# Kernel optimization log

Hardware: AMD Instinct MI355X
Metric: run time of the kernel (lower is better)

## Reference

```python
import jax, jax.numpy as jnp
import numpy as np

NUM_EXPERTS = 64
TOP_K = 2

def setup_inputs() -> dict:
    key = jax.random.key(0)
    k1, k2, k3, k4 = jax.random.split(key, 4)
    B, N, C, E = 4, 4096, 2048, NUM_EXPERTS
    x = jax.random.normal(k1, (B, N, C), dtype=jnp.float32)
    routing_context = jax.random.normal(k2, (B, C), dtype=jnp.float32)
    # Linear(C, E, bias=False) and Linear(C, C, bias=False), torch layout (out, in)
    gate_w = jax.random.normal(k3, (E, C), dtype=jnp.float32) * (1.0 / np.sqrt(C))
    ctx_w = jax.random.normal(k4, (C, C), dtype=jnp.float32) * (1.0 / np.sqrt(C))
    return {"x": x, "routing_context": routing_context, "gate_w": gate_w, "ctx_w": ctx_w}

def reference(x, routing_context, gate_w, ctx_w):
    B, N, C = x.shape
    T = B * N
    E = gate_w.shape[0]
    # context_proj(routing_context): (B,C) @ (C,C)^T -> broadcast over N
    ctx = routing_context @ ctx_w.T                      # (B, C)
    x_routing = (x + ctx[:, None, :]).reshape(T, C)      # (T, C)
    logits = x_routing @ gate_w.T                        # (T, E)
    top_vals, top_idx = jax.lax.top_k(logits, TOP_K)     # (T, K) each
    top_weights = jax.nn.softmax(top_vals, axis=-1)      # (T, K)
    probs = jax.nn.softmax(logits, axis=-1)              # (T, E)
    importance = probs.sum(axis=0) / T                   # (E,)
    # load: fraction of tokens that pick each expert in their top-k
    load = jnp.zeros((E,), dtype=probs.dtype).at[top_idx.reshape(-1)].add(1.0) / T
    aux_loss = E * (importance * load).sum()
    return top_idx, top_weights, aux_loss
```

## Files before the change

### kernel.cpp

```cpp
#include <hip/hip_runtime.h>
#include <math.h>

#define T_TOKENS 16384
#define C_DIM    2048
#define N_SEQ    4096
#define E_EXP    64
#define NSLICE   4
#define KSLICE   512
#define EPB      1024
#define GN       131072

typedef __attribute__((ext_vector_type(8))) short  short8;
typedef __attribute__((ext_vector_type(4))) float  floatx4;

__device__ __forceinline__ void splitv(float v, ushort& h, ushort& m, ushort& l) {
    unsigned u = __float_as_uint(v);
    h = (ushort)(u >> 16);
    float f1 = v - __uint_as_float(u & 0xffff0000u);
    unsigned u1 = __float_as_uint(f1);
    m = (ushort)(u1 >> 16);
    float f2 = f1 - __uint_as_float(u1 & 0xffff0000u);
    l = (ushort)(__float_as_uint(f2) >> 16);
}

__device__ __forceinline__ void splitpack8(const float4& a, const float4& b,
                                           short8& h, short8& m, short8& l) {
    ushort hh, mm, ll;
    splitv(a.x, hh, mm, ll); h[0] = hh; m[0] = mm; l[0] = ll;
    splitv(a.y, hh, mm, ll); h[1] = hh; m[1] = mm; l[1] = ll;
    splitv(a.z, hh, mm, ll); h[2] = hh; m[2] = mm; l[2] = ll;
    splitv(a.w, hh, mm, ll); h[3] = hh; m[3] = mm; l[3] = ll;
    splitv(b.x, hh, mm, ll); h[4] = hh; m[4] = mm; l[4] = ll;
    splitv(b.y, hh, mm, ll); h[5] = hh; m[5] = mm; l[5] = ll;
    splitv(b.z, hh, mm, ll); h[6] = hh; m[6] = mm; l[6] = ll;
    splitv(b.w, hh, mm, ll); h[7] = hh; m[7] = mm; l[7] = ll;
}

__device__ __forceinline__ void split3rne(float v, ushort& h, ushort& m, ushort& l) {
    unsigned u = __float_as_uint(v);
    unsigned r = (u + 0x7fffu + ((u >> 16) & 1u)) >> 16;
    h = (ushort)r;
    float e1 = v - __uint_as_float(r << 16);
    u = __float_as_uint(e1);
    r = (u + 0x7fffu + ((u >> 16) & 1u)) >> 16;
    m = (ushort)r;
    float e2 = e1 - __uint_as_float(r << 16);
    l = (ushort)(__float_as_uint(e2) >> 16);
}

__global__ __launch_bounds__(256) void ctx_kernel(
    const float* __restrict__ rc, const float* __restrict__ ctx_w,
    float* __restrict__ ctx_out)
{
    const int w    = threadIdx.x >> 6;
    const int lane = threadIdx.x & 63;
    const int o    = blockIdx.x * 4 + w;
    const int b    = o >> 11;
    const int j    = o & 2047;

    const float4* wr = (const float4*)(ctx_w + (size_t)j * C_DIM);
    const float4* rr = (const float4*)(rc + (size_t)b * C_DIM);
    float s = 0.f;
#pragma unroll
    for (int it = 0; it < 8; ++it) {
        float4 a = wr[it * 64 + lane];
        float4 c = rr[it * 64 + lane];
        s += a.x * c.x + a.y * c.y + a.z * c.z + a.w * c.w;
    }
#pragma unroll
    for (int off = 32; off; off >>= 1) s += __shfl_xor(s, off, 64);
    if (lane == 0) ctx_out[b * C_DIM + j] = s;
}

__global__ __launch_bounds__(256) void prep_kernel(
    const float* __restrict__ gw, const float* __restrict__ ctx,
    ushort* __restrict__ gsp, float* __restrict__ cl)
{
    if (blockIdx.x < 512) {
        const int idx  = blockIdx.x * 256 + threadIdx.x;
        const int j    = idx & 7;
        const int e    = (idx >> 3) & 63;
        const int koct = idx >> 9;
        float g = gw[(size_t)e * C_DIM + koct * 8 + j];
        ushort h, m, l;
        split3rne(g, h, m, l);
        gsp[idx]          = h;
        gsp[GN + idx]     = m;
        gsp[2 * GN + idx] = l;
    } else {
        const int lane = threadIdx.x & 63;
        const int pk   = (blockIdx.x - 512) * 4 + (threadIdx.x >> 6);
        const int b    = pk >> 6;
        const int e    = pk & 63;
        const float4* wr = (const float4*)(gw + (size_t)e * C_DIM);
        const float4* cr = (const float4*)(ctx + (size_t)b * C_DIM);
        float s = 0.f;
#pragma unroll
        for (int it = 0; it < 8; ++it) {
            float4 a = wr[it * 64 + lane];
            float4 c = cr[it * 64 + lane];
            s += a.x * c.x + a.y * c.y + a.z * c.z + a.w * c.w;
        }
#pragma unroll
        for (int off = 32; off; off >>= 1) s += __shfl_xor(s, off, 64);
        if (lane == 0) cl[pk] = s;
    }
}

__global__ __launch_bounds__(256) void gemm_mfma_kernel(
    const float* __restrict__ x, const ushort* __restrict__ gsp,
    float* __restrict__ P)
{
    const int tid   = threadIdx.x;
    const int wv    = tid >> 6;
    const int lane  = tid & 63;
    const int l15   = lane & 15;
    const int quad  = lane >> 4;
    const int tile  = blockIdx.x & 127;
    const int slice = blockIdx.x >> 7;
    const int tw    = tile * 128 + wv * 32;
    const int cbase = slice * KSLICE;

    floatx4 acc[2][4];
#pragma unroll
    for (int s = 0; s < 2; ++s)
#pragma unroll
        for (int nt = 0; nt < 4; ++nt) acc[s][nt] = (floatx4){0.f, 0.f, 0.f, 0.f};

    const float* xr0 = x + (size_t)(tw + l15) * C_DIM + cbase + quad * 8;
    const float* xr1 = xr0 + (size_t)16 * C_DIM;
    const ushort* bb = gsp + ((size_t)((cbase >> 3) + quad) * 64 + l15) * 8;

#pragma unroll 2
    for (int ks = 0; ks < KSLICE / 32; ++ks) {
        float4 a00 = *(const float4*)(xr0 + ks * 32);
        float4 a01 = *(const float4*)(xr0 + ks * 32 + 4);
        float4 a10 = *(const float4*)(xr1 + ks * 32);
        float4 a11 = *(const float4*)(xr1 + ks * 32 + 4);
        short8 ah0, am0, al0, ah1, am1, al1;
        splitpack8(a00, a01, ah0, am0, al0);
        splitpack8(a10, a11, ah1, am1, al1);

        const ushort* bks = bb + (size_t)ks * 4 * 64 * 8;
#pragma unroll
        for (int nt = 0; nt < 4; ++nt) {
            const ushort* bp_ = bks + (size_t)(16 * nt) * 8;
            short8 bh = *(const short8*)(bp_);
            short8 bm = *(const short8*)(bp_ + GN);
            short8 bl = *(const short8*)(bp_ + 2 * (size_t)GN);
            acc[0][nt] = __builtin_amdgcn_mfma_f32_16x16x32_bf16(ah0, bh, acc[0][nt], 0, 0, 0);
            acc[0][nt] = __builtin_amdgcn_mfma_f32_16x16x32_bf16(ah0, bm, acc[0][nt], 0, 0, 0);
            acc[0][nt] = __builtin_amdgcn_mfma_f32_16x16x32_bf16(am0, bh, acc[0][nt], 0, 0, 0);
            acc[0][nt] = __builtin_amdgcn_mfma_f32_16x16x32_bf16(ah0, bl, acc[0][nt], 0, 0, 0);
            acc[0][nt] = __builtin_amdgcn_mfma_f32_16x16x32_bf16(al0, bh, acc[0][nt], 0, 0, 0);
            acc[0][nt] = __builtin_amdgcn_mfma_f32_16x16x32_bf16(am0, bm, acc[0][nt], 0, 0, 0);
            acc[1][nt] = __builtin_amdgcn_mfma_f32_16x16x32_bf16(ah1, bh, acc[1][nt], 0, 0, 0);
            acc[1][nt] = __builtin_amdgcn_mfma_f32_16x16x32_bf16(ah1, bm, acc[1][nt], 0, 0, 0);
            acc[1][nt] = __builtin_amdgcn_mfma_f32_16x16x32_bf16(am1, bh, acc[1][nt], 0, 0, 0);
            acc[1][nt] = __builtin_amdgcn_mfma_f32_16x16x32_bf16(ah1, bl, acc[1][nt], 0, 0, 0);
            acc[1][nt] = __builtin_amdgcn_mfma_f32_16x16x32_bf16(al1, bh, acc[1][nt], 0, 0, 0);
            acc[1][nt] = __builtin_amdgcn_mfma_f32_16x16x32_bf16(am1, bm, acc[1][nt], 0, 0, 0);
        }
    }

    float* Ps = P + ((size_t)slice * T_TOKENS + tw) * E_EXP;
#pragma unroll
    for (int s = 0; s < 2; ++s)
#pragma unroll
        for (int nt = 0; nt < 4; ++nt)
#pragma unroll
            for (int r = 0; r < 4; ++r)
                Ps[(size_t)(s * 16 + quad * 4 + r) * E_EXP + 16 * nt + l15] =
                    acc[s][nt][r];
}

__global__ __launch_bounds__(256) void epilogue_kernel(
    const float* __restrict__ P, const float* __restrict__ cl,
    float* __restrict__ out, float* __restrict__ bp)
{
    __shared__ float red[4][128];

    const int tid  = threadIdx.x;
    const int wv   = tid >> 6;
    const int lane = tid & 63;
    const int t0   = blockIdx.x * (T_TOKENS / EPB);
    const float clv = cl[(t0 >> 12) * 64 + lane];

    float imp_acc = 0.f, cnt_acc = 0.f;

    for (int tt = 0; tt < 4; ++tt) {
        const int t = t0 + wv * 4 + tt;
        float v = clv;
#pragma unroll
        for (int s = 0; s < NSLICE; ++s)
            v += P[((size_t)s * T_TOKENS + t) * E_EXP + lane];

        const float p = expf(v);
        float v1 = v;  int i1 = lane;
        float v2 = -INFINITY; int i2 = 0x7fffffff;
        float s = p;
#pragma unroll
        for (int off = 32; off; off >>= 1) {
            float ov1 = __shfl_xor(v1, off, 64);
            int   oi1 = __shfl_xor(i1, off, 64);
            float ov2 = __shfl_xor(v2, off, 64);
            int   oi2 = __shfl_xor(i2, off, 64);
            s += __shfl_xor(s, off, 64);
            const bool aw = (ov1 < v1) || (ov1 == v1 && i1 < oi1);
            const float lv = aw ? ov1 : v1;  const int li = aw ? oi1 : i1;
            const float wv2 = aw ? v2 : ov2; const int wi = aw ? i2 : oi2;
            if (!aw) { v1 = ov1; i1 = oi1; }
            const bool sw = (wv2 < lv) || (wv2 == lv && li < wi);
            v2 = sw ? lv : wv2; i2 = sw ? li : wi;
        }

        imp_acc += p / s;
        if (lane == i1 || lane == i2) cnt_acc += 1.f;

        if (lane == 0) {
            const float e2 = expf(v2 - v1);
            out[2 * t]     = (float)i1;
            out[2 * t + 1] = (float)i2;
            out[2 * T_TOKENS + 2 * t]     = 1.f / (1.f + e2);
            out[2 * T_TOKENS + 2 * t + 1] = e2 / (1.f + e2);
        }
    }

    red[wv][lane]      = imp_acc;
    red[wv][64 + lane] = cnt_acc;
    __syncthreads();
    if (tid < 128) {
        float s = red[0][tid] + red[1][tid] + red[2][tid] + red[3][tid];
        bp[(size_t)blockIdx.x * 128 + tid] = s;
    }
}

__global__ __launch_bounds__(1024) void aux_kernel(
    const float* __restrict__ bp, int nb, float* __restrict__ out_aux)
{
    __shared__ float4 red[32][32];
    const int tid = threadIdx.x;
    const int c4  = tid & 31;
    const int grp = tid >> 5;

    const float4* bp4 = (const float4*)bp;
    float4 s = make_float4(0.f, 0.f, 0.f, 0.f);
    for (int r = grp; r < nb; r += 32) {
        float4 v = bp4[(size_t)r * 32 + c4];
        s.x += v.x; s.y += v.y; s.z += v.z; s.w += v.w;
    }
    red[grp][c4] = s;
    __syncthreads();

    if (tid < 32) {
        float4 t = make_float4(0.f, 0.f, 0.f, 0.f);
#pragma unroll
        for (int g = 0; g < 32; ++g) {
            float4 v = red[g][tid];
            t.x += v.x; t.y += v.y; t.z += v.z; t.w += v.w;
        }
        red[0][tid] = t;
    }
    __syncthreads();

    if (tid < 16) {
        float4 a = red[0][tid];
        float4 b = red[0][tid + 16];
        float v = a.x * b.x + a.y * b.y + a.z * b.z + a.w * b.w;
#pragma unroll
        for (int off = 8; off; off >>= 1) v += __shfl_xor(v, off, 64);
        if (tid == 0)
            out_aux[0] = (float)E_EXP * v / ((float)T_TOKENS * (float)T_TOKENS);
    }
}

#define TM    64
#define FKC   64
#define FLSTR 68
__global__ __launch_bounds__(256) void router_fused_kernel(
    const float* __restrict__ x, const float* __restrict__ gate_w,
    const float* __restrict__ ctx, float* __restrict__ out,
    float* __restrict__ bp)
{
    __shared__ float xs[TM][FLSTR];
    __shared__ float gs[E_EXP][FLSTR];
    __shared__ float ls[TM][FLSTR];
    __shared__ float red[4][128];

    const int tid = threadIdx.x;
    const int eg  = tid & 15;
    const int tg  = tid >> 4;
    const int t0  = blockIdx.x * TM;
    const int b   = t0 / N_SEQ;
    const int sr  = tid >> 4;
    const int scg = tid & 15;
    const float* ctx_row = ctx + (size_t)b * C_DIM;

    float4 acc[4][4];
#pragma unroll
    for (int i = 0; i < 4; ++i)
#pragma unroll
        for (int j = 0; j < 4; ++j) acc[i][j] = make_float4(0.f, 0.f, 0.f, 0.f);

    float4 px[4], pg[4], pc;
    auto prefetch = [&](int kc) {
        const int c0 = kc * FKC + scg * 4;
        pc = *(const float4*)(ctx_row + c0);
#pragma unroll
        for (int i = 0; i < 4; ++i) {
            px[i] = *(const float4*)(x + (size_t)(t0 + sr + 16 * i) * C_DIM + c0);
            pg[i] = *(const float4*)(gate_w + (size_t)(sr + 16 * i) * C_DIM + c0);
        }
    };

    prefetch(0);
    const int NCHUNK = C_DIM / FKC;
    for (int kc = 0; kc < NCHUNK; ++kc) {
        __syncthreads();
#pragma unroll
        for (int i = 0; i < 4; ++i) {
            float4 v = px[i];
            v.x += pc.x; v.y += pc.y; v.z += pc.z; v.w += pc.w;
            *(float4*)&xs[sr + 16 * i][scg * 4] = v;
            *(float4*)&gs[sr + 16 * i][scg * 4] = pg[i];
        }
        __syncthreads();
        if (kc + 1 < NCHUNK) prefetch(kc + 1);
#pragma unroll
        for (int cc = 0; cc < FKC; cc += 4) {
            float4 xv[4], gv[4];
#pragma unroll
            for (int i = 0; i < 4; ++i) xv[i] = *(const float4*)&xs[tg + 16 * i][cc];
#pragma unroll
            for (int j = 0; j < 4; ++j) gv[j] = *(const float4*)&gs[eg + 16 * j][cc];
#pragma unroll
            for (int i = 0; i < 4; ++i)
#pragma unroll
                for (int j = 0; j < 4; ++j) {
                    acc[i][j].x = fmaf(xv[i].x, gv[j].x, acc[i][j].x);
                    acc[i][j].y = fmaf(xv[i].y, gv[j].y, acc[i][j].y);
                    acc[i][j].z = fmaf(xv[i].z, gv[j].z, acc[i][j].z);
                    acc[i][j].w = fmaf(xv[i].w, gv[j].w, acc[i][j].w);
                }
        }
    }

    __syncthreads();
#pragma unroll
    for (int i = 0; i < 4; ++i)
#pragma unroll
        for (int j = 0; j < 4; ++j)
            ls[tg + 16 * i][eg + 16 * j] =
                (acc[i][j].x + acc[i][j].y) + (acc[i][j].z + acc[i][j].w);
    __syncthreads();

    const int wv   = tid >> 6;
    const int lane = tid & 63;
    float imp_acc = 0.f, cnt_acc = 0.f;

    for (int tt = 0; tt < 16; ++tt) {
        const int tokL = wv * 16 + tt;
        const float v = ls[tokL][lane];
        const float p = expf(v);
        float v1 = v;  int i1 = lane;
        float v2 = -INFINITY; int i2 = 0x7fffffff;
        float s = p;
#pragma unroll
        for (int off = 32; off; off >>= 1) {
            float ov1 = __shfl_xor(v1, off, 64);
            int   oi1 = __shfl_xor(i1, off, 64);
            float ov2 = __shfl_xor(v2, off, 64);
            int   oi2 = __shfl_xor(i2, off, 64);
            s += __shfl_xor(s, off, 64);
            const bool aw = (ov1 < v1) || (ov1 == v1 && i1 < oi1);
            const float lv = aw ? ov1 : v1;  const int li = aw ? oi1 : i1;
            const float wv2 = aw ? v2 : ov2; const int wi = aw ? i2 : oi2;
            if (!aw) { v1 = ov1; i1 = oi1; }
            const bool sw = (wv2 < lv) || (wv2 == lv && li < wi);
            v2 = sw ? lv : wv2; i2 = sw ? li : wi;
        }
        imp_acc += p / s;
        if (lane == i1 || lane == i2) cnt_acc += 1.f;
        if (lane == 0) {
            const int t = t0 + tokL;
            const float e2 = expf(v2 - v1);
            out[2 * t]     = (float)i1;
            out[2 * t + 1] = (float)i2;
            out[2 * T_TOKENS + 2 * t]     = 1.f / (1.f + e2);
            out[2 * T_TOKENS + 2 * t + 1] = e2 / (1.f + e2);
        }
    }

    red[wv][lane]      = imp_acc;
    red[wv][64 + lane] = cnt_acc;
    __syncthreads();
    if (tid < 128) {
        float s = red[0][tid] + red[1][tid] + red[2][tid] + red[3][tid];
        bp[(size_t)blockIdx.x * 128 + tid] = s;
    }
}

extern "C" void kernel_launch(void* const* d_in, const int* in_sizes, int n_in,
                              void* d_out, int out_size, void* d_ws, size_t ws_size,
                              hipStream_t stream)
{
    (void)in_sizes; (void)n_in; (void)out_size;
    const float* x      = (const float*)d_in[0];
    const float* rc     = (const float*)d_in[1];
    const float* gate_w = (const float*)d_in[2];
    const float* ctx_w  = (const float*)d_in[3];
    float* out = (float*)d_out;

    float*  ctx = (float*)d_ws;
    float*  cl  = ctx + 8192;
    float*  bp  = cl + 256;
    float*  P   = bp + (size_t)EPB * 128;
    ushort* gsp = (ushort*)(P + (size_t)NSLICE * T_TOKENS * E_EXP);

    const size_t need =
        (8192 + 256 + (size_t)EPB * 128 + (size_t)NSLICE * T_TOKENS * E_EXP)
            * sizeof(float)
        + (size_t)3 * GN * sizeof(ushort);

    ctx_kernel<<<2048, 256, 0, stream>>>(rc, ctx_w, ctx);
    if (ws_size >= need) {
        prep_kernel<<<576, 256, 0, stream>>>(gate_w, ctx, gsp, cl);
        gemm_mfma_kernel<<<128 * NSLICE, 256, 0, stream>>>(x, gsp, P);
        epilogue_kernel<<<EPB, 256, 0, stream>>>(P, cl, out, bp);
        aux_kernel<<<1, 1024, 0, stream>>>(bp, EPB, out + 2 * 2 * T_TOKENS);
    } else {
        router_fused_kernel<<<256, 256, 0, stream>>>(x, gate_w, ctx, out, bp);
        aux_kernel<<<1, 1024, 0, stream>>>(bp, 256, out + 2 * 2 * T_TOKENS);
    }
}
```

Before: 245.7 us.

## Fuse five launches into three: merge ctx/prep, gemm/cl, epilogue/aux

Folds the ctx projection and the gate-weight bf16 split into one pre kernel, and moves the per-batch context-logit dot products into extra blocks of the GEMM launch. The final aux-loss reduction now runs in the last epilogue block, found through an atomic counter with threadfences. This removes two kernel launches and their inter-kernel gaps. The cost is a global atomic per epilogue block and a serial tail reduction done by one 256-thread block.

```diff
diff --git a/kernel.cpp b/kernel.cpp
--- a/kernel.cpp
+++ b/kernel.cpp
@@ -48,35 +48,14 @@
     l = (ushort)(__float_as_uint(e2) >> 16);
 }
 
-__global__ __launch_bounds__(256) void ctx_kernel(
+__global__ __launch_bounds__(256) void pre_kernel(
     const float* __restrict__ rc, const float* __restrict__ ctx_w,
-    float* __restrict__ ctx_out)
-{
-    const int w    = threadIdx.x >> 6;
-    const int lane = threadIdx.x & 63;
-    const int o    = blockIdx.x * 4 + w;
-    const int b    = o >> 11;
-    const int j    = o & 2047;
-
-    const float4* wr = (const float4*)(ctx_w + (size_t)j * C_DIM);
-    const float4* rr = (const float4*)(rc + (size_t)b * C_DIM);
-    float s = 0.f;
-#pragma unroll
-    for (int it = 0; it < 8; ++it) {
-        float4 a = wr[it * 64 + lane];
-        float4 c = rr[it * 64 + lane];
-        s += a.x * c.x + a.y * c.y + a.z * c.z + a.w * c.w;
-    }
-#pragma unroll
-    for (int off = 32; off; off >>= 1) s += __shfl_xor(s, off, 64);
-    if (lane == 0) ctx_out[b * C_DIM + j] = s;
-}
-
-__global__ __launch_bounds__(256) void prep_kernel(
-    const float* __restrict__ gw, const float* __restrict__ ctx,
-    ushort* __restrict__ gsp, float* __restrict__ cl)
-{
-    if (blockIdx.x < 512) {
+    const float* __restrict__ gw, float* __restrict__ ctx_out,
+    ushort* __restrict__ gsp, unsigned* __restrict__ counter)
+{
+    if (counter != nullptr && blockIdx.x == 0 && threadIdx.x == 0) *counter = 0u;
+
+    if (gsp != nullptr && blockIdx.x < 512) {
         const int idx  = blockIdx.x * 256 + threadIdx.x;
         const int j    = idx & 7;
         const int e    = (idx >> 3) & 63;
@@ -87,9 +66,36 @@
         gsp[idx]          = h;
         gsp[GN + idx]     = m;
         gsp[2 * GN + idx] = l;
-    } else {
+    }
+
+    const int w    = threadIdx.x >> 6;
+    const int lane = threadIdx.x & 63;
+    const int o    = blockIdx.x * 4 + w;
+    const int b    = o >> 11;
+    const int j    = o & 2047;
+
+    const float4* wr = (const float4*)(ctx_w + (size_t)j * C_DIM);
+    const float4* rr = (const float4*)(rc + (size_t)b * C_DIM);
+    float s = 0.f;
+#pragma unroll
+    for (int it = 0; it < 8; ++it) {
+        float4 a = wr[it * 64 + lane];
+        float4 c = rr[it * 64 + lane];
+        s += a.x * c.x + a.y * c.y + a.z * c.z + a.w * c.w;
+    }
+#pragma unroll
+    for (int off = 32; off; off >>= 1) s += __shfl_xor(s, off, 64);
+    if (lane == 0) ctx_out[b * C_DIM + j] = s;
+}
+
+__global__ __launch_bounds__(256) void gemm_cl_kernel(
+    const float* __restrict__ x, const ushort* __restrict__ gsp,
+    const float* __restrict__ gw, const float* __restrict__ ctx,
+    float* __restrict__ P, float* __restrict__ cl)
+{
+    if (blockIdx.x >= 128 * NSLICE) {
         const int lane = threadIdx.x & 63;
-        const int pk   = (blockIdx.x - 512) * 4 + (threadIdx.x >> 6);
+        const int pk   = (blockIdx.x - 128 * NSLICE) * 4 + (threadIdx.x >> 6);
         const int b    = pk >> 6;
         const int e    = pk & 63;
         const float4* wr = (const float4*)(gw + (size_t)e * C_DIM);
@@ -104,13 +110,9 @@
 #pragma unroll
         for (int off = 32; off; off >>= 1) s += __shfl_xor(s, off, 64);
         if (lane == 0) cl[pk] = s;
-    }
-}
-
-__global__ __launch_bounds__(256) void gemm_mfma_kernel(
-    const float* __restrict__ x, const ushort* __restrict__ gsp,
-    float* __restrict__ P)
-{
+        return;
+    }
+
     const int tid   = threadIdx.x;
     const int wv    = tid >> 6;
     const int lane  = tid & 63;
@@ -174,11 +176,14 @@
                     acc[s][nt][r];
 }
 
-__global__ __launch_bounds__(256) void epilogue_kernel(
+__global__ __launch_bounds__(256) void epilogue_aux_kernel(
     const float* __restrict__ P, const float* __restrict__ cl,
-    float* __restrict__ out, float* __restrict__ bp)
-{
-    __shared__ float red[4][128];
+    float* __restrict__ out, float* __restrict__ bp,
+    unsigned* __restrict__ counter, float* __restrict__ out_aux)
+{
+    __shared__ float  red[4][128];
+    __shared__ float4 fred[8][32];
+    __shared__ int    lastflag;
 
     const int tid  = threadIdx.x;
     const int wv   = tid >> 6;
@@ -233,6 +238,46 @@
         float s = red[0][tid] + red[1][tid] + red[2][tid] + red[3][tid];
         bp[(size_t)blockIdx.x * 128 + tid] = s;
     }
+
+    __threadfence();
+    __syncthreads();
+    if (tid == 0)
+        lastflag = (atomicAdd(counter, 1u) == (unsigned)(EPB - 1)) ? 1 : 0;
+    __syncthreads();
+    if (!lastflag) return;
+
+    __threadfence();
+    const float4* bp4 = (const float4*)bp;
+    const int c4  = tid & 31;
+    const int grp = tid >> 5;
+    float4 s4 = make_float4(0.f, 0.f, 0.f, 0.f);
+    for (int r = grp; r < EPB; r += 8) {
+        float4 v = bp4[(size_t)r * 32 + c4];
+        s4.x += v.x; s4.y += v.y; s4.z += v.z; s4.w += v.w;
+    }
+    fred[grp][c4] = s4;
+    __syncthreads();
+
+    if (tid < 32) {
+        float4 t = make_float4(0.f, 0.f, 0.f, 0.f);
+#pragma unroll
+        for (int g = 0; g < 8; ++g) {
+            float4 v = fred[g][tid];
+            t.x += v.x; t.y += v.y; t.z += v.z; t.w += v.w;
+        }
+        fred[0][tid] = t;
+    }
+    __syncthreads();
+
+    if (tid < 16) {
+        float4 a = fred[0][tid];
+        float4 b = fred[0][tid + 16];
+        float v = a.x * b.x + a.y * b.y + a.z * b.z + a.w * b.w;
+#pragma unroll
+        for (int off = 8; off; off >>= 1) v += __shfl_xor(v, off, 64);
+        if (tid == 0)
+            out_aux[0] = (float)E_EXP * v / ((float)T_TOKENS * (float)T_TOKENS);
+    }
 }
 
 __global__ __launch_bounds__(1024) void aux_kernel(
@@ -416,19 +461,20 @@
     float*  bp  = cl + 256;
     float*  P   = bp + (size_t)EPB * 128;
     ushort* gsp = (ushort*)(P + (size_t)NSLICE * T_TOKENS * E_EXP);
+    unsigned* counter = (unsigned*)(gsp + (size_t)3 * GN);
 
     const size_t need =
         (8192 + 256 + (size_t)EPB * 128 + (size_t)NSLICE * T_TOKENS * E_EXP)
             * sizeof(float)
-        + (size_t)3 * GN * sizeof(ushort);
-
-    ctx_kernel<<<2048, 256, 0, stream>>>(rc, ctx_w, ctx);
+        + (size_t)3 * GN * sizeof(ushort) + sizeof(unsigned);
+
     if (ws_size >= need) {
-        prep_kernel<<<576, 256, 0, stream>>>(gate_w, ctx, gsp, cl);
-        gemm_mfma_kernel<<<128 * NSLICE, 256, 0, stream>>>(x, gsp, P);
-        epilogue_kernel<<<EPB, 256, 0, stream>>>(P, cl, out, bp);
-        aux_kernel<<<1, 1024, 0, stream>>>(bp, EPB, out + 2 * 2 * T_TOKENS);
+        pre_kernel<<<2048, 256, 0, stream>>>(rc, ctx_w, gate_w, ctx, gsp, counter);
+        gemm_cl_kernel<<<128 * NSLICE + 64, 256, 0, stream>>>(x, gsp, gate_w, ctx, P, cl);
+        epilogue_aux_kernel<<<EPB, 256, 0, stream>>>(P, cl, out, bp, counter,
+                                                     out + 2 * 2 * T_TOKENS);
     } else {
+        pre_kernel<<<2048, 256, 0, stream>>>(rc, ctx_w, gate_w, ctx, nullptr, nullptr);
         router_fused_kernel<<<256, 256, 0, stream>>>(x, gate_w, ctx, out, bp);
         aux_kernel<<<1, 1024, 0, stream>>>(bp, 256, out + 2 * 2 * T_TOKENS);
     }
```

After: 335.5 us. +36.6%, slower.
